# Kernel optimization log

Measured on AMD Instinct MI355X. Metric: run time of the kernel, lower is better.

The kernel has to match this reference:

```python
import jax, jax.numpy as jnp
import numpy as np

B, C, H, W = 32, 256, 32, 32
HID, NPATH = 128, 4


def setup_inputs() -> dict:
    key = jax.random.key(0)
    ks = jax.random.split(key, 16)
    s = lambda *sh: 1.0 / np.sqrt(sh[-1])
    inp = {
        "lidar": jax.random.normal(ks[0], (B, C, H, W), jnp.float32),
        "hsi": jax.random.normal(ks[1], (B, C, H, W), jnp.float32),
        "x": jax.random.normal(ks[2], (B, C, H, W), jnp.float32),
        # shared Cross_Self_attention params
        "Wq": jax.random.normal(ks[3], (C, C), jnp.float32) * s(C, C),
        "bq": jnp.zeros((C,), jnp.float32),
        "Wk": jax.random.normal(ks[4], (C, C), jnp.float32) * s(C, C),
        "bk": jnp.zeros((C,), jnp.float32),
        "Wv": jax.random.normal(ks[5], (C, C), jnp.float32) * s(C, C),
        "bv": jnp.zeros((C,), jnp.float32),
        # 1x1 conv: [out=C, in=2C]
        "conv_w": jax.random.normal(ks[6], (C, 2 * C), jnp.float32) * s(C, 2 * C),
        "conv_b": jnp.zeros((C,), jnp.float32),
        # router MLP
        "r_w1": jax.random.normal(ks[7], (HID, 2 * C), jnp.float32) * s(HID, 2 * C),
        "r_b1": jnp.zeros((HID,), jnp.float32),
        "r_w2": jax.random.normal(ks[8], (NPATH, HID), jnp.float32) * s(NPATH, HID),
        "r_b2": jnp.zeros((NPATH,), jnp.float32),
    }
    return inp


def _cross_self_attn(xq, yv, Wq, bq, Wk, bk, Wv, bv):
    # xq, yv: [b, s, c]
    q = xq @ Wq.T + bq
    k = xq @ Wk.T + bk
    v = yv @ Wv.T + bv
    probs = jax.nn.softmax(jnp.einsum("bsc,btc->bst", q, k), axis=-1)  # [b,s,s]
    return jnp.einsum("bst,btc->bsc", probs, q * v)  # bilinear value Q*V


def reference(lidar, hsi, x, Wq, bq, Wk, bk, Wv, bv, conv_w, conv_b, r_w1, r_b1, r_w2, r_b2):
    b, c, h, w = lidar.shape
    # Router: concat channels, spatial mean pool, MLP, sigmoid
    g = jnp.concatenate([lidar, hsi], axis=1).mean(axis=(2, 3))  # [b, 2c]
    path_prob = jax.nn.sigmoid(jax.nn.relu(g @ r_w1.T + r_b1) @ r_w2.T + r_b2)

    l = lidar.reshape(b, c, h * w).transpose(0, 2, 1)  # b (h w) c
    hh = hsi.reshape(b, c, h * w).transpose(0, 2, 1)

    h_emb = _cross_self_attn(l, hh, Wq, bq, Wk, bk, Wv, bv)  # [b, hw, c]
    l_emb = _cross_self_attn(hh, l, Wq, bq, Wk, bk, Wv, bv)

    h_emb = h_emb.transpose(0, 2, 1).reshape(b, c, h, w)
    l_emb = l_emb.transpose(0, 2, 1).reshape(b, c, h, w)

    cat = jnp.concatenate([l_emb, h_emb], axis=1)  # [b, 2c, h, w]
    emb = jnp.einsum("bihw,oi->bohw", cat, conv_w) + conv_b[None, :, None, None] + x
    return emb, path_prob
```

## Files before the change

kernel.cpp:

```cpp
#include <hip/hip_runtime.h>
#include <stdint.h>

typedef unsigned short u16;
typedef unsigned int u32;
typedef _Float16 f16;
typedef _Float16 f16x8 __attribute__((ext_vector_type(8)));
typedef _Float16 f16x4 __attribute__((ext_vector_type(4)));
typedef float f32x4 __attribute__((ext_vector_type(4)));

#define B_ 32
#define C_ 256
#define S_ 1024

__global__ __launch_bounds__(256) void k_mlp(
    const float* __restrict__ g,
    const float* __restrict__ w1, const float* __restrict__ b1,
    const float* __restrict__ w2, const float* __restrict__ b2,
    float* __restrict__ out)
{
    int b = blockIdx.x, tid = threadIdx.x;
    __shared__ float sg[512];
    __shared__ float sh[128];
    sg[tid]     = g[b*512 + tid]       * (1.0f/1024.0f);
    sg[tid+256] = g[b*512 + 256 + tid] * (1.0f/1024.0f);
    __syncthreads();
    if (tid < 128){
        float a = b1[tid];
        const float* w = w1 + (size_t)tid*512;
        #pragma unroll 4
        for (int k = 0; k < 512; k += 4){
            float4 wv = *(const float4*)(w + k);
            a += sg[k]*wv.x + sg[k+1]*wv.y + sg[k+2]*wv.z + sg[k+3]*wv.w;
        }
        sh[tid] = fmaxf(a, 0.f);
    }
    __syncthreads();
    if (tid < 4){
        float a = b2[tid];
        const float* w = w2 + (size_t)tid*128;
        for (int k = 0; k < 128; ++k) a += sh[k]*w[k];
        out[(size_t)8388608 + b*4 + tid] = 1.f/(1.f+expf(-a));
    }
}

__global__ __launch_bounds__(256) void k_cvtw(
    const float* __restrict__ Wq, const float* __restrict__ Wk,
    const float* __restrict__ Wv, const float* __restrict__ cw,
    f16* __restrict__ Wqf, f16* __restrict__ Wkf,
    f16* __restrict__ Wvf, f16* __restrict__ cwf)
{
    int i = (blockIdx.x*256 + threadIdx.x) * 4;
    const float* src; f16* dst; int off;
    if (i < 65536){ src = Wq; dst = Wqf; off = i; }
    else if (i < 131072){ src = Wk; dst = Wkf; off = i - 65536; }
    else if (i < 196608){ src = Wv; dst = Wvf; off = i - 131072; }
    else { src = cw; dst = cwf; off = i - 196608; }
    float4 v = *(const float4*)(src + off);
    f16x4 r = { (f16)v.x, (f16)v.y, (f16)v.z, (f16)v.w };
    *(f16x4*)(dst + off) = r;
}

__global__ __launch_bounds__(256) void k_cvt(
    const float* __restrict__ lidar, const float* __restrict__ hsi,
    f16* __restrict__ lidT, f16* __restrict__ hsiT,
    float* __restrict__ g)
{
    int z = blockIdx.z, which = z >> 5, b = z & 31;
    const float* src = (which ? hsi : lidar) + (size_t)b*C_*S_;
    f16* dst = (which ? hsiT : lidT) + (size_t)b*S_*C_;
    int tid = threadIdx.x;
    int c4 = blockIdx.y*64 + (tid&15)*4;
    int s4 = blockIdx.x*64 + (tid>>4)*4;
    float4 m[4];
    #pragma unroll
    for (int r = 0; r < 4; ++r) m[r] = *(const float4*)(src + (size_t)(c4+r)*S_ + s4);
    f16x4 t0 = { (f16)m[0].x, (f16)m[1].x, (f16)m[2].x, (f16)m[3].x };
    f16x4 t1 = { (f16)m[0].y, (f16)m[1].y, (f16)m[2].y, (f16)m[3].y };
    f16x4 t2 = { (f16)m[0].z, (f16)m[1].z, (f16)m[2].z, (f16)m[3].z };
    f16x4 t3 = { (f16)m[0].w, (f16)m[1].w, (f16)m[2].w, (f16)m[3].w };
    *(f16x4*)(dst + (size_t)(s4+0)*C_ + c4) = t0;
    *(f16x4*)(dst + (size_t)(s4+1)*C_ + c4) = t1;
    *(f16x4*)(dst + (size_t)(s4+2)*C_ + c4) = t2;
    *(f16x4*)(dst + (size_t)(s4+3)*C_ + c4) = t3;
    float ps[4];
    #pragma unroll
    for (int r = 0; r < 4; ++r){
        ps[r] = m[r].x + m[r].y + m[r].z + m[r].w;
        ps[r] += __shfl_xor(ps[r], 16, 64);
        ps[r] += __shfl_xor(ps[r], 32, 64);
    }
    __shared__ float sred[4][64];
    int wv = tid>>6, lane = tid&63;
    if ((lane>>4) == 0){
        #pragma unroll
        for (int r = 0; r < 4; ++r) sred[wv][(lane&15)*4 + r] = ps[r];
    }
    __syncthreads();
    if (tid < 64){
        float v = sred[0][tid] + sred[1][tid] + sred[2][tid] + sred[3][tid];
        atomicAdd(&g[b*512 + which*256 + blockIdx.y*64 + tid], v);
    }
}

__global__ __launch_bounds__(256) void k_qkv(
    const f16* __restrict__ lidT, const f16* __restrict__ hsiT,
    const f16* __restrict__ Wqf, const f16* __restrict__ Wkf, const f16* __restrict__ Wvf,
    const float* __restrict__ bq, const float* __restrict__ bk, const float* __restrict__ bv,
    f16* __restrict__ Qf_l, f16* __restrict__ Kf_l,
    f16* __restrict__ Qf_h, f16* __restrict__ Kf_h,
    f16* __restrict__ Qt_l, f16* __restrict__ Qt_h,
    f16* __restrict__ Vt_l, f16* __restrict__ Vt_h)
{
    int z = blockIdx.z, combo = z >> 5, b = z & 31, ww = combo % 3;
    const f16* In = ((combo < 3) ? lidT : hsiT) + (size_t)b*S_*C_;
    const f16* Wf = (ww==0) ? Wqf : (ww==1) ? Wkf : Wvf;
    const float* bias = (ww==0) ? bq : (ww==1) ? bk : bv;
    int s0 = blockIdx.x*64, o0 = blockIdx.y*64;
    int tid = threadIdx.x, w = tid>>6, lane = tid&63, quad = lane>>4, l15 = lane&15;

    __shared__ __align__(16) f16 sA[64*72];
    __shared__ __align__(16) f16 sB[64*72];

    f32x4 D[4];
    #pragma unroll
    for (int i = 0; i < 4; ++i) D[i] = (f32x4){0.f,0.f,0.f,0.f};

    int row = tid>>2, c16 = (tid&3)*16;
    for (int c0 = 0; c0 < 256; c0 += 64){
        __syncthreads();
        *(f16x8*)&sA[row*72 + c16]     = *(const f16x8*)(In + (size_t)(s0+row)*C_ + c0 + c16);
        *(f16x8*)&sA[row*72 + c16 + 8] = *(const f16x8*)(In + (size_t)(s0+row)*C_ + c0 + c16 + 8);
        *(f16x8*)&sB[row*72 + c16]     = *(const f16x8*)(Wf + (size_t)(o0+row)*C_ + c0 + c16);
        *(f16x8*)&sB[row*72 + c16 + 8] = *(const f16x8*)(Wf + (size_t)(o0+row)*C_ + c0 + c16 + 8);
        __syncthreads();
        #pragma unroll
        for (int sub = 0; sub < 2; ++sub){
            f16x8 a = *(const f16x8*)&sA[(w*16+l15)*72 + sub*32 + quad*8];
            #pragma unroll
            for (int bt = 0; bt < 4; ++bt){
                f16x8 bb = *(const f16x8*)&sB[(bt*16+l15)*72 + sub*32 + quad*8];
                D[bt] = __builtin_amdgcn_mfma_f32_16x16x32_f16(a, bb, D[bt], 0,0,0);
            }
        }
    }
    float bi[4];
    #pragma unroll
    for (int bt = 0; bt < 4; ++bt) bi[bt] = bias[o0 + bt*16 + l15];

    if (ww == 0){
        f16* F = ((combo==0) ? Qf_l : Qf_h) + (size_t)b*S_*C_;
        #pragma unroll
        for (int bt = 0; bt < 4; ++bt)
            #pragma unroll
            for (int r = 0; r < 4; ++r)
                F[(size_t)(s0 + w*16 + quad*4 + r)*C_ + o0 + bt*16 + l15] = (f16)(D[bt][r] + bi[bt]);
    } else if (ww == 1){
        f16* F = ((combo==1) ? Kf_l : Kf_h) + (size_t)b*S_*C_;
        #pragma unroll
        for (int bt = 0; bt < 4; ++bt)
            #pragma unroll
            for (int r = 0; r < 4; ++r)
                F[(size_t)(s0 + w*16 + quad*4 + r)*C_ + o0 + bt*16 + l15] = (f16)(D[bt][r] + bi[bt]);
    }
    if (ww != 1){
        __syncthreads();
        #pragma unroll
        for (int bt = 0; bt < 4; ++bt)
            #pragma unroll
            for (int r = 0; r < 4; ++r)
                sA[(bt*16+l15)*72 + w*16 + quad*4 + r] = (f16)(D[bt][r] + bi[bt]);
        __syncthreads();
        f16* T = (combo==0) ? Qt_l : (combo==3) ? Qt_h : (combo==2) ? Vt_l : Vt_h;
        T += (size_t)b*C_*S_;
        int o_r = tid>>2, s16b = (tid&3)*16;
        *(f16x8*)(T + (size_t)(o0+o_r)*S_ + s0 + s16b)     = *(const f16x8*)&sA[o_r*72 + s16b];
        *(f16x8*)(T + (size_t)(o0+o_r)*S_ + s0 + s16b + 8) = *(const f16x8*)&sA[o_r*72 + s16b + 8];
    }
}

__global__ __launch_bounds__(256) void k_qv(
    const f16* __restrict__ Qt_l, const f16* __restrict__ Qt_h,
    const f16* __restrict__ Vt_l, const f16* __restrict__ Vt_h,
    f16* __restrict__ QVT1, f16* __restrict__ QVT2)
{
    size_t idx = (size_t)(blockIdx.x*256 + threadIdx.x) * 8;
    f16x8 a = *(const f16x8*)(Qt_l+idx);
    f16x8 b = *(const f16x8*)(Vt_h+idx);
    *(f16x8*)(QVT1+idx) = a*b;
    f16x8 c = *(const f16x8*)(Qt_h+idx);
    f16x8 d = *(const f16x8*)(Vt_l+idx);
    *(f16x8*)(QVT2+idx) = c*d;
}

__global__ __launch_bounds__(256, 2) void k_attn(
    const f16* __restrict__ Qf_l, const f16* __restrict__ Kf_l,
    const f16* __restrict__ Qf_h, const f16* __restrict__ Kf_h,
    const f16* __restrict__ QVT1, const f16* __restrict__ QVT2,
    f16* __restrict__ cat)
{
    int inst = blockIdx.y;
    int b = inst >> 1, which = inst & 1;
    const f16* Qf  = (which ? Qf_h : Qf_l) + (size_t)b*S_*C_;
    const f16* Kf  = (which ? Kf_h : Kf_l) + (size_t)b*S_*C_;
    const f16* QVT = (which ? QVT2 : QVT1) + (size_t)b*C_*S_;
    f16* outp = cat + (size_t)b*S_*512 + (which ? 0 : 256);
    int s0 = blockIdx.x*64;
    int tid = threadIdx.x, w = tid>>6, lane = tid&63, quad = lane>>4, l15 = lane&15;

    __shared__ __align__(16) f16 sK[64*264];
    __shared__ __align__(16) f16 sV[256*72];
    __shared__ __align__(16) f16 sPw[4][16*66];

    f16x8 qa[8];
    {
        const f16* qrow = Qf + (size_t)(s0 + w*16 + l15)*C_ + quad*8;
        #pragma unroll
        for (int i = 0; i < 8; ++i) qa[i] = *(const f16x8*)(qrow + i*32);
    }
    float mrun[4], lrun[4];
    #pragma unroll
    for (int r = 0; r < 4; ++r){ mrun[r] = -1e30f; lrun[r] = 0.f; }
    f32x4 pacc[16];
    #pragma unroll
    for (int i = 0; i < 16; ++i) pacc[i] = (f32x4){0.f,0.f,0.f,0.f};

    for (int tt = 0; tt < 16; ++tt){
        int t0 = tt*64;
        __syncthreads();
        #pragma unroll
        for (int p = 0; p < 8; ++p){
            int idx = p*256 + tid;
            int row = idx >> 5, c8 = (idx & 31)*8;
            *(f16x8*)&sK[row*264 + c8] = *(const f16x8*)(Kf + (size_t)(t0+row)*C_ + c8);
        }
        #pragma unroll
        for (int p = 0; p < 8; ++p){
            int idx = p*256 + tid;
            int row = idx >> 3, t8 = (idx & 7)*8;
            *(f16x8*)&sV[row*72 + t8] = *(const f16x8*)(QVT + (size_t)row*S_ + t0 + t8);
        }
        __syncthreads();

        f32x4 sacc[4];
        #pragma unroll
        for (int bt = 0; bt < 4; ++bt) sacc[bt] = (f32x4){0.f,0.f,0.f,0.f};
        #pragma unroll
        for (int ks = 0; ks < 8; ++ks){
            #pragma unroll
            for (int bt = 0; bt < 4; ++bt){
                f16x8 kb = *(const f16x8*)&sK[(bt*16+l15)*264 + ks*32 + quad*8];
                sacc[bt] = __builtin_amdgcn_mfma_f32_16x16x32_f16(qa[ks], kb, sacc[bt], 0,0,0);
            }
        }

        float alpha[4], lsum[4];
        #pragma unroll
        for (int r = 0; r < 4; ++r){
            float tm = fmaxf(fmaxf(sacc[0][r], sacc[1][r]), fmaxf(sacc[2][r], sacc[3][r]));
            #pragma unroll
            for (int off = 1; off < 16; off <<= 1) tm = fmaxf(tm, __shfl_xor(tm, off, 64));
            float mn = fmaxf(mrun[r], tm);
            alpha[r] = __expf(mrun[r] - mn);
            mrun[r] = mn;
            float acc = 0.f;
            #pragma unroll
            for (int bt = 0; bt < 4; ++bt){
                float p = __expf(sacc[bt][r] - mn);
                sPw[w][(quad*4+r)*66 + bt*16 + l15] = (f16)p;
                acc += p;
            }
            #pragma unroll
            for (int off = 1; off < 16; off <<= 1) acc += __shfl_xor(acc, off, 64);
            lsum[r] = acc;
            lrun[r] = lrun[r]*alpha[r] + lsum[r];
        }
        #pragma unroll
        for (int cf = 0; cf < 16; ++cf)
            #pragma unroll
            for (int r = 0; r < 4; ++r) pacc[cf][r] *= alpha[r];

        f16x8 pa0 = *(const f16x8*)&sPw[w][l15*66 + quad*8];
        f16x8 pa1 = *(const f16x8*)&sPw[w][l15*66 + 32 + quad*8];

        #pragma unroll
        for (int cf = 0; cf < 16; ++cf){
            f16x8 vb0 = *(const f16x8*)&sV[(cf*16+l15)*72 + quad*8];
            f16x8 vb1 = *(const f16x8*)&sV[(cf*16+l15)*72 + 32 + quad*8];
            pacc[cf] = __builtin_amdgcn_mfma_f32_16x16x32_f16(pa0, vb0, pacc[cf], 0,0,0);
            pacc[cf] = __builtin_amdgcn_mfma_f32_16x16x32_f16(pa1, vb1, pacc[cf], 0,0,0);
        }
    }

    #pragma unroll
    for (int r = 0; r < 4; ++r){
        int s = w*16 + quad*4 + r;
        float rl = 1.f / lrun[r];
        #pragma unroll
        for (int cf = 0; cf < 16; ++cf)
            outp[(size_t)(s0+s)*512 + cf*16 + l15] = (f16)(pacc[cf][r] * rl);
    }
}

__global__ __launch_bounds__(256) void k_conv(
    const f16* __restrict__ cat, const f16* __restrict__ cwf,
    const float* __restrict__ cb, const float* __restrict__ x,
    float* __restrict__ out)
{
    int b = blockIdx.z;
    int s0 = blockIdx.x*64, o0 = blockIdx.y*64;
    int tid = threadIdx.x, w = tid>>6, lane = tid&63, quad = lane>>4, l15 = lane&15;

    __shared__ __align__(16) f16 sA[64*72];
    __shared__ __align__(16) f16 sB[64*72];

    f32x4 D[4];
    #pragma unroll
    for (int i = 0; i < 4; ++i) D[i] = (f32x4){0.f,0.f,0.f,0.f};

    const f16* catb = cat + (size_t)b*S_*512;
    int row = tid>>2, c16 = (tid&3)*16;
    for (int i0 = 0; i0 < 512; i0 += 64){
        __syncthreads();
        *(f16x8*)&sA[row*72 + c16]     = *(const f16x8*)(cwf + (size_t)(o0+row)*512 + i0 + c16);
        *(f16x8*)&sA[row*72 + c16 + 8] = *(const f16x8*)(cwf + (size_t)(o0+row)*512 + i0 + c16 + 8);
        *(f16x8*)&sB[row*72 + c16]     = *(const f16x8*)(catb + (size_t)(s0+row)*512 + i0 + c16);
        *(f16x8*)&sB[row*72 + c16 + 8] = *(const f16x8*)(catb + (size_t)(s0+row)*512 + i0 + c16 + 8);
        __syncthreads();
        #pragma unroll
        for (int sub = 0; sub < 2; ++sub){
            f16x8 a = *(const f16x8*)&sA[(w*16+l15)*72 + sub*32 + quad*8];
            #pragma unroll
            for (int bt = 0; bt < 4; ++bt){
                f16x8 bb = *(const f16x8*)&sB[(bt*16+l15)*72 + sub*32 + quad*8];
                D[bt] = __builtin_amdgcn_mfma_f32_16x16x32_f16(a, bb, D[bt], 0,0,0);
            }
        }
    }
    #pragma unroll
    for (int r = 0; r < 4; ++r){
        int o_loc = w*16 + quad*4 + r;
        float cbv = cb[o0 + o_loc];
        size_t base = (size_t)b*C_*S_ + (size_t)(o0+o_loc)*S_ + s0;
        #pragma unroll
        for (int bt = 0; bt < 4; ++bt){
            size_t a = base + bt*16 + l15;
            out[a] = D[bt][r] + cbv + x[a];
        }
    }
}

extern "C" void kernel_launch(void* const* d_in, const int* in_sizes, int n_in,
                              void* d_out, int out_size, void* d_ws, size_t ws_size,
                              hipStream_t stream)
{
    const float* lidar = (const float*)d_in[0];
    const float* hsi   = (const float*)d_in[1];
    const float* x     = (const float*)d_in[2];
    const float* Wq = (const float*)d_in[3];  const float* bq = (const float*)d_in[4];
    const float* Wk = (const float*)d_in[5];  const float* bk = (const float*)d_in[6];
    const float* Wv = (const float*)d_in[7];  const float* bv = (const float*)d_in[8];
    const float* cw = (const float*)d_in[9];  const float* cb = (const float*)d_in[10];
    const float* rw1 = (const float*)d_in[11]; const float* rb1 = (const float*)d_in[12];
    const float* rw2 = (const float*)d_in[13]; const float* rb2 = (const float*)d_in[14];
    float* outF = (float*)d_out;
    char* ws = (char*)d_ws;
    const size_t M = 1ull<<20;

    f16* lidT = (f16*)(ws +   0*M);
    f16* hsiT = (f16*)(ws +  16*M);
    f16* Qf_l = (f16*)(ws +  32*M);
    f16* Kf_l = (f16*)(ws +  48*M);
    f16* Qf_h = (f16*)(ws +  64*M);
    f16* Kf_h = (f16*)(ws +  80*M);
    f16* Qt_l = (f16*)(ws +  96*M);
    f16* Qt_h = (f16*)(ws + 112*M);
    f16* cat  = (f16*)(ws + 128*M);
    float* g  = (float*)(ws + 160*M);
    f16* Wqf  = (f16*)(ws + 161*M);
    f16* Wkf  = (f16*)(ws + 161*M + 131072);
    f16* Wvf  = (f16*)(ws + 161*M + 262144);
    f16* cwf  = (f16*)(ws + 161*M + 393216);
    f16* QVT1 = lidT;
    f16* QVT2 = hsiT;
    f16* Vt_l = (f16*)d_out;
    f16* Vt_h = (f16*)d_out + 8388608;

    hipMemsetAsync(g, 0, 4096*sizeof(float), stream);
    k_cvtw<<<320, 256, 0, stream>>>(Wq, Wk, Wv, cw, Wqf, Wkf, Wvf, cwf);
    k_cvt<<<dim3(16,4,64), 256, 0, stream>>>(lidar, hsi, lidT, hsiT, g);
    k_mlp<<<32, 256, 0, stream>>>(g, rw1, rb1, rw2, rb2, outF);
    k_qkv<<<dim3(16,4,192), 256, 0, stream>>>(lidT, hsiT, Wqf, Wkf, Wvf, bq, bk, bv,
                                              Qf_l, Kf_l, Qf_h, Kf_h, Qt_l, Qt_h, Vt_l, Vt_h);
    k_qv<<<4096, 256, 0, stream>>>(Qt_l, Qt_h, Vt_l, Vt_h, QVT1, QVT2);
    k_attn<<<dim3(16,64), 256, 0, stream>>>(Qf_l, Kf_l, Qf_h, Kf_h, QVT1, QVT2, cat);
    k_conv<<<dim3(16,4,32), 256, 0, stream>>>(cat, cwf, cb, x, outF);
}
```

Baseline: 407.4 us.

## Rework attention with 32x32 MFMA split tiles and enlarge QKV/conv GEMM tiles

The attention kernel now uses 32x32x16 MFMA, with waves splitting a 64x64 score tile two ways over query rows and key columns. K fragments are loaded straight from global memory into registers instead of going through shared memory. Softmax max and sum are reduced across waves through shared memory, and the output is staged through LDS for coalesced stores. The QKV and conv GEMMs double their tile along one dimension (128 rows) so each wave issues two MFMA chains per B fragment, halving grid size and increasing register use. In exchange, the attention kernel adds several extra block-wide barriers per key tile and carries more register pressure.

```diff
diff --git a/kernel.cpp b/kernel.cpp
--- a/kernel.cpp
+++ b/kernel.cpp
@@ -7,6 +7,7 @@
 typedef _Float16 f16x8 __attribute__((ext_vector_type(8)));
 typedef _Float16 f16x4 __attribute__((ext_vector_type(4)));
 typedef float f32x4 __attribute__((ext_vector_type(4)));
+typedef float f32x16 __attribute__((ext_vector_type(16)));
 
 #define B_ 32
 #define C_ 256
@@ -115,31 +116,38 @@
     const f16* In = ((combo < 3) ? lidT : hsiT) + (size_t)b*S_*C_;
     const f16* Wf = (ww==0) ? Wqf : (ww==1) ? Wkf : Wvf;
     const float* bias = (ww==0) ? bq : (ww==1) ? bk : bv;
-    int s0 = blockIdx.x*64, o0 = blockIdx.y*64;
+    int s0 = blockIdx.x*128, o0 = blockIdx.y*64;
     int tid = threadIdx.x, w = tid>>6, lane = tid&63, quad = lane>>4, l15 = lane&15;
 
-    __shared__ __align__(16) f16 sA[64*72];
+    __shared__ __align__(16) f16 sA[128*72];
     __shared__ __align__(16) f16 sB[64*72];
 
-    f32x4 D[4];
-    #pragma unroll
-    for (int i = 0; i < 4; ++i) D[i] = (f32x4){0.f,0.f,0.f,0.f};
-
-    int row = tid>>2, c16 = (tid&3)*16;
+    f32x4 D[2][4];
+    #pragma unroll
+    for (int h = 0; h < 2; ++h)
+        #pragma unroll
+        for (int i = 0; i < 4; ++i) D[h][i] = (f32x4){0.f,0.f,0.f,0.f};
+
+    int rowA = tid>>1, cA = (tid&1)*32;
+    int rowB = tid>>2, cB = (tid&3)*16;
     for (int c0 = 0; c0 < 256; c0 += 64){
         __syncthreads();
-        *(f16x8*)&sA[row*72 + c16]     = *(const f16x8*)(In + (size_t)(s0+row)*C_ + c0 + c16);
-        *(f16x8*)&sA[row*72 + c16 + 8] = *(const f16x8*)(In + (size_t)(s0+row)*C_ + c0 + c16 + 8);
-        *(f16x8*)&sB[row*72 + c16]     = *(const f16x8*)(Wf + (size_t)(o0+row)*C_ + c0 + c16);
-        *(f16x8*)&sB[row*72 + c16 + 8] = *(const f16x8*)(Wf + (size_t)(o0+row)*C_ + c0 + c16 + 8);
+        #pragma unroll
+        for (int j = 0; j < 4; ++j)
+            *(f16x8*)&sA[rowA*72 + cA + 8*j] = *(const f16x8*)(In + (size_t)(s0+rowA)*C_ + c0 + cA + 8*j);
+        #pragma unroll
+        for (int j = 0; j < 2; ++j)
+            *(f16x8*)&sB[rowB*72 + cB + 8*j] = *(const f16x8*)(Wf + (size_t)(o0+rowB)*C_ + c0 + cB + 8*j);
         __syncthreads();
         #pragma unroll
         for (int sub = 0; sub < 2; ++sub){
-            f16x8 a = *(const f16x8*)&sA[(w*16+l15)*72 + sub*32 + quad*8];
+            f16x8 a0 = *(const f16x8*)&sA[(w*16+l15)*72 + sub*32 + quad*8];
+            f16x8 a1 = *(const f16x8*)&sA[((w+4)*16+l15)*72 + sub*32 + quad*8];
             #pragma unroll
             for (int bt = 0; bt < 4; ++bt){
                 f16x8 bb = *(const f16x8*)&sB[(bt*16+l15)*72 + sub*32 + quad*8];
-                D[bt] = __builtin_amdgcn_mfma_f32_16x16x32_f16(a, bb, D[bt], 0,0,0);
+                D[0][bt] = __builtin_amdgcn_mfma_f32_16x16x32_f16(a0, bb, D[0][bt], 0,0,0);
+                D[1][bt] = __builtin_amdgcn_mfma_f32_16x16x32_f16(a1, bb, D[1][bt], 0,0,0);
             }
         }
     }
@@ -147,34 +155,33 @@
     #pragma unroll
     for (int bt = 0; bt < 4; ++bt) bi[bt] = bias[o0 + bt*16 + l15];
 
-    if (ww == 0){
-        f16* F = ((combo==0) ? Qf_l : Qf_h) + (size_t)b*S_*C_;
-        #pragma unroll
-        for (int bt = 0; bt < 4; ++bt)
-            #pragma unroll
-            for (int r = 0; r < 4; ++r)
-                F[(size_t)(s0 + w*16 + quad*4 + r)*C_ + o0 + bt*16 + l15] = (f16)(D[bt][r] + bi[bt]);
-    } else if (ww == 1){
-        f16* F = ((combo==1) ? Kf_l : Kf_h) + (size_t)b*S_*C_;
-        #pragma unroll
-        for (int bt = 0; bt < 4; ++bt)
-            #pragma unroll
-            for (int r = 0; r < 4; ++r)
-                F[(size_t)(s0 + w*16 + quad*4 + r)*C_ + o0 + bt*16 + l15] = (f16)(D[bt][r] + bi[bt]);
+    if (ww != 2){
+        f16* F = (ww==0) ? ((combo==0) ? Qf_l : Qf_h) : ((combo==1) ? Kf_l : Kf_h);
+        F += (size_t)b*S_*C_;
+        #pragma unroll
+        for (int h = 0; h < 2; ++h)
+            #pragma unroll
+            for (int bt = 0; bt < 4; ++bt)
+                #pragma unroll
+                for (int r = 0; r < 4; ++r)
+                    F[(size_t)(s0 + h*64 + w*16 + quad*4 + r)*C_ + o0 + bt*16 + l15] = (f16)(D[h][bt][r] + bi[bt]);
     }
     if (ww != 1){
         __syncthreads();
         #pragma unroll
-        for (int bt = 0; bt < 4; ++bt)
-            #pragma unroll
-            for (int r = 0; r < 4; ++r)
-                sA[(bt*16+l15)*72 + w*16 + quad*4 + r] = (f16)(D[bt][r] + bi[bt]);
+        for (int h = 0; h < 2; ++h)
+            #pragma unroll
+            for (int bt = 0; bt < 4; ++bt)
+                #pragma unroll
+                for (int r = 0; r < 4; ++r)
+                    sA[(bt*16+l15)*136 + h*64 + w*16 + quad*4 + r] = (f16)(D[h][bt][r] + bi[bt]);
         __syncthreads();
         f16* T = (combo==0) ? Qt_l : (combo==3) ? Qt_h : (combo==2) ? Vt_l : Vt_h;
         T += (size_t)b*C_*S_;
-        int o_r = tid>>2, s16b = (tid&3)*16;
-        *(f16x8*)(T + (size_t)(o0+o_r)*S_ + s0 + s16b)     = *(const f16x8*)&sA[o_r*72 + s16b];
-        *(f16x8*)(T + (size_t)(o0+o_r)*S_ + s0 + s16b + 8) = *(const f16x8*)&sA[o_r*72 + s16b + 8];
+        int o_r = tid>>2, sc = (tid&3)*32;
+        #pragma unroll
+        for (int j = 0; j < 4; ++j)
+            *(f16x8*)(T + (size_t)(o0+o_r)*S_ + s0 + sc + 8*j) = *(const f16x8*)&sA[o_r*136 + sc + 8*j];
     }
 }
 
@@ -205,99 +212,112 @@
     const f16* QVT = (which ? QVT2 : QVT1) + (size_t)b*C_*S_;
     f16* outp = cat + (size_t)b*S_*512 + (which ? 0 : 256);
     int s0 = blockIdx.x*64;
-    int tid = threadIdx.x, w = tid>>6, lane = tid&63, quad = lane>>4, l15 = lane&15;
-
-    __shared__ __align__(16) f16 sK[64*264];
+    int tid = threadIdx.x, w = tid>>6, lane = tid&63;
+    int l31 = lane&31, b5 = lane>>5;
+    int sh2 = w&1, hf = w>>1;
+
     __shared__ __align__(16) f16 sV[256*72];
-    __shared__ __align__(16) f16 sPw[4][16*66];
-
-    f16x8 qa[8];
+    __shared__ __align__(16) f16 sP[64*72];
+    __shared__ float sRm[2][64], sRl[2][64];
+    __shared__ float sSt[64][2];
+
+    f16x8 qB[16];
     {
-        const f16* qrow = Qf + (size_t)(s0 + w*16 + l15)*C_ + quad*8;
-        #pragma unroll
-        for (int i = 0; i < 8; ++i) qa[i] = *(const f16x8*)(qrow + i*32);
-    }
-    float mrun[4], lrun[4];
-    #pragma unroll
-    for (int r = 0; r < 4; ++r){ mrun[r] = -1e30f; lrun[r] = 0.f; }
-    f32x4 pacc[16];
-    #pragma unroll
-    for (int i = 0; i < 16; ++i) pacc[i] = (f32x4){0.f,0.f,0.f,0.f};
+        const f16* qbase = Qf + (size_t)(s0 + 32*sh2 + l31)*C_ + b5*8;
+        #pragma unroll
+        for (int k = 0; k < 16; ++k) qB[k] = *(const f16x8*)(qbase + k*16);
+    }
+    if (tid < 64){ sSt[tid][0] = -1e30f; sSt[tid][1] = 0.f; }
+
+    f32x16 pacc[4];
+    #pragma unroll
+    for (int i = 0; i < 4; ++i) pacc[i] = (f32x16)(0.f);
+
+    const f16* kbase = Kf + (size_t)(32*hf + l31)*C_ + b5*8;
+    int smy = 32*sh2 + l31;
 
     for (int tt = 0; tt < 16; ++tt){
         int t0 = tt*64;
         __syncthreads();
         #pragma unroll
         for (int p = 0; p < 8; ++p){
-            int idx = p*256 + tid;
-            int row = idx >> 5, c8 = (idx & 31)*8;
-            *(f16x8*)&sK[row*264 + c8] = *(const f16x8*)(Kf + (size_t)(t0+row)*C_ + c8);
-        }
-        #pragma unroll
-        for (int p = 0; p < 8; ++p){
-            int idx = p*256 + tid;
-            int row = idx >> 3, t8 = (idx & 7)*8;
+            int idx = p*256 + tid; int row = idx>>3, t8 = (idx&7)*8;
             *(f16x8*)&sV[row*72 + t8] = *(const f16x8*)(QVT + (size_t)row*S_ + t0 + t8);
         }
-        __syncthreads();
-
-        f32x4 sacc[4];
-        #pragma unroll
-        for (int bt = 0; bt < 4; ++bt) sacc[bt] = (f32x4){0.f,0.f,0.f,0.f};
-        #pragma unroll
-        for (int ks = 0; ks < 8; ++ks){
-            #pragma unroll
-            for (int bt = 0; bt < 4; ++bt){
-                f16x8 kb = *(const f16x8*)&sK[(bt*16+l15)*264 + ks*32 + quad*8];
-                sacc[bt] = __builtin_amdgcn_mfma_f32_16x16x32_f16(qa[ks], kb, sacc[bt], 0,0,0);
+        f16x8 kA[16];
+        {
+            const f16* kb = kbase + (size_t)t0*C_;
+            #pragma unroll
+            for (int k = 0; k < 16; ++k) kA[k] = *(const f16x8*)(kb + k*16);
+        }
+        __syncthreads();
+
+        f32x16 St = (f32x16)(0.f);
+        #pragma unroll
+        for (int k = 0; k < 16; ++k)
+            St = __builtin_amdgcn_mfma_f32_32x32x16_f16(kA[k], qB[k], St, 0,0,0);
+
+        float tmax = St[0];
+        #pragma unroll
+        for (int i = 1; i < 16; ++i) tmax = fmaxf(tmax, St[i]);
+        tmax = fmaxf(tmax, __shfl_xor(tmax, 32, 64));
+        if (lane < 32) sRm[hf][32*sh2 + lane] = tmax;
+        __syncthreads();
+
+        float mo = sSt[smy][0];
+        float mn = fmaxf(mo, fmaxf(sRm[0][smy], sRm[1][smy]));
+        float p16[16];
+        float ls = 0.f;
+        #pragma unroll
+        for (int i = 0; i < 16; ++i){ p16[i] = __expf(St[i] - mn); ls += p16[i]; }
+        #pragma unroll
+        for (int g = 0; g < 4; ++g){
+            f16x4 pk = { (f16)p16[4*g], (f16)p16[4*g+1], (f16)p16[4*g+2], (f16)p16[4*g+3] };
+            *(f16x4*)&sP[smy*72 + 32*hf + 8*g + 4*b5] = pk;
+        }
+        ls += __shfl_xor(ls, 32, 64);
+        if (lane < 32) sRl[hf][32*sh2 + lane] = ls;
+        __syncthreads();
+
+        float alpha = __expf(mo - mn);
+        if (hf == 0 && lane < 32){
+            float ln = sSt[smy][1]*alpha + sRl[0][smy] + sRl[1][smy];
+            sSt[smy][0] = mn; sSt[smy][1] = ln;
+        }
+        #pragma unroll
+        for (int ct = 0; ct < 4; ++ct)
+            #pragma unroll
+            for (int i = 0; i < 16; ++i) pacc[ct][i] *= alpha;
+
+        #pragma unroll
+        for (int kp = 0; kp < 4; ++kp){
+            f16x8 pB = *(const f16x8*)&sP[smy*72 + kp*16 + b5*8];
+            #pragma unroll
+            for (int ct = 0; ct < 4; ++ct){
+                f16x8 vA = *(const f16x8*)&sV[(128*hf + 32*ct + l31)*72 + kp*16 + b5*8];
+                pacc[ct] = __builtin_amdgcn_mfma_f32_32x32x16_f16(vA, pB, pacc[ct], 0,0,0);
             }
         }
-
-        float alpha[4], lsum[4];
-        #pragma unroll
-        for (int r = 0; r < 4; ++r){
-            float tm = fmaxf(fmaxf(sacc[0][r], sacc[1][r]), fmaxf(sacc[2][r], sacc[3][r]));
-            #pragma unroll
-            for (int off = 1; off < 16; off <<= 1) tm = fmaxf(tm, __shfl_xor(tm, off, 64));
-            float mn = fmaxf(mrun[r], tm);
-            alpha[r] = __expf(mrun[r] - mn);
-            mrun[r] = mn;
-            float acc = 0.f;
-            #pragma unroll
-            for (int bt = 0; bt < 4; ++bt){
-                float p = __expf(sacc[bt][r] - mn);
-                sPw[w][(quad*4+r)*66 + bt*16 + l15] = (f16)p;
-                acc += p;
-            }
-            #pragma unroll
-            for (int off = 1; off < 16; off <<= 1) acc += __shfl_xor(acc, off, 64);
-            lsum[r] = acc;
-            lrun[r] = lrun[r]*alpha[r] + lsum[r];
-        }
-        #pragma unroll
-        for (int cf = 0; cf < 16; ++cf)
-            #pragma unroll
-            for (int r = 0; r < 4; ++r) pacc[cf][r] *= alpha[r];
-
-        f16x8 pa0 = *(const f16x8*)&sPw[w][l15*66 + quad*8];
-        f16x8 pa1 = *(const f16x8*)&sPw[w][l15*66 + 32 + quad*8];
-
-        #pragma unroll
-        for (int cf = 0; cf < 16; ++cf){
-            f16x8 vb0 = *(const f16x8*)&sV[(cf*16+l15)*72 + quad*8];
-            f16x8 vb1 = *(const f16x8*)&sV[(cf*16+l15)*72 + 32 + quad*8];
-            pacc[cf] = __builtin_amdgcn_mfma_f32_16x16x32_f16(pa0, vb0, pacc[cf], 0,0,0);
-            pacc[cf] = __builtin_amdgcn_mfma_f32_16x16x32_f16(pa1, vb1, pacc[cf], 0,0,0);
-        }
-    }
-
-    #pragma unroll
-    for (int r = 0; r < 4; ++r){
-        int s = w*16 + quad*4 + r;
-        float rl = 1.f / lrun[r];
-        #pragma unroll
-        for (int cf = 0; cf < 16; ++cf)
-            outp[(size_t)(s0+s)*512 + cf*16 + l15] = (f16)(pacc[cf][r] * rl);
+    }
+
+    __syncthreads();
+    float rl = 1.f / sSt[smy][1];
+    f16* sE = sV;
+    #pragma unroll
+    for (int ct = 0; ct < 4; ++ct)
+        #pragma unroll
+        for (int i = 0; i < 16; ++i){
+            int cl = 128*hf + 32*ct + (i&3) + 8*(i>>2) + 4*b5;
+            sE[(32*sh2 + l31)*264 + cl] = (f16)(pacc[ct][i] * rl);
+        }
+    __syncthreads();
+    {
+        int s = tid>>2;
+        #pragma unroll
+        for (int i = 0; i < 8; ++i){
+            int c8 = ((tid&3) + 4*i)*8;
+            *(f16x8*)(outp + (size_t)(s0+s)*512 + c8) = *(const f16x8*)&sE[s*264 + c8];
+        }
     }
 }
 
@@ -307,46 +327,55 @@
     float* __restrict__ out)
 {
     int b = blockIdx.z;
-    int s0 = blockIdx.x*64, o0 = blockIdx.y*64;
+    int s0 = blockIdx.x*64, o0 = blockIdx.y*128;
     int tid = threadIdx.x, w = tid>>6, lane = tid&63, quad = lane>>4, l15 = lane&15;
 
-    __shared__ __align__(16) f16 sA[64*72];
+    __shared__ __align__(16) f16 sA[128*72];
     __shared__ __align__(16) f16 sB[64*72];
 
-    f32x4 D[4];
-    #pragma unroll
-    for (int i = 0; i < 4; ++i) D[i] = (f32x4){0.f,0.f,0.f,0.f};
+    f32x4 D[2][4];
+    #pragma unroll
+    for (int h = 0; h < 2; ++h)
+        #pragma unroll
+        for (int i = 0; i < 4; ++i) D[h][i] = (f32x4){0.f,0.f,0.f,0.f};
 
     const f16* catb = cat + (size_t)b*S_*512;
-    int row = tid>>2, c16 = (tid&3)*16;
+    int rowA = tid>>1, iA = (tid&1)*32;
+    int rowB = tid>>2, iB = (tid&3)*16;
     for (int i0 = 0; i0 < 512; i0 += 64){
         __syncthreads();
-        *(f16x8*)&sA[row*72 + c16]     = *(const f16x8*)(cwf + (size_t)(o0+row)*512 + i0 + c16);
-        *(f16x8*)&sA[row*72 + c16 + 8] = *(const f16x8*)(cwf + (size_t)(o0+row)*512 + i0 + c16 + 8);
-        *(f16x8*)&sB[row*72 + c16]     = *(const f16x8*)(catb + (size_t)(s0+row)*512 + i0 + c16);
-        *(f16x8*)&sB[row*72 + c16 + 8] = *(const f16x8*)(catb + (size_t)(s0+row)*512 + i0 + c16 + 8);
+        #pragma unroll
+        for (int j = 0; j < 4; ++j)
+            *(f16x8*)&sA[rowA*72 + iA + 8*j] = *(const f16x8*)(cwf + (size_t)(o0+rowA)*512 + i0 + iA + 8*j);
+        #pragma unroll
+        for (int j = 0; j < 2; ++j)
+            *(f16x8*)&sB[rowB*72 + iB + 8*j] = *(const f16x8*)(catb + (size_t)(s0+rowB)*512 + i0 + iB + 8*j);
         __syncthreads();
         #pragma unroll
         for (int sub = 0; sub < 2; ++sub){
-            f16x8 a = *(const f16x8*)&sA[(w*16+l15)*72 + sub*32 + quad*8];
+            f16x8 a0 = *(const f16x8*)&sA[(w*16+l15)*72 + sub*32 + quad*8];
+            f16x8 a1 = *(const f16x8*)&sA[((w+4)*16+l15)*72 + sub*32 + quad*8];
             #pragma unroll
             for (int bt = 0; bt < 4; ++bt){
                 f16x8 bb = *(const f16x8*)&sB[(bt*16+l15)*72 + sub*32 + quad*8];
-                D[bt] = __builtin_amdgcn_mfma_f32_16x16x32_f16(a, bb, D[bt], 0,0,0);
+                D[0][bt] = __builtin_amdgcn_mfma_f32_16x16x32_f16(a0, bb, D[0][bt], 0,0,0);
+                D[1][bt] = __builtin_amdgcn_mfma_f32_16x16x32_f16(a1, bb, D[1][bt], 0,0,0);
             }
         }
     }
     #pragma unroll
-    for (int r = 0; r < 4; ++r){
-        int o_loc = w*16 + quad*4 + r;
-        float cbv = cb[o0 + o_loc];
-        size_t base = (size_t)b*C_*S_ + (size_t)(o0+o_loc)*S_ + s0;
-        #pragma unroll
-        for (int bt = 0; bt < 4; ++bt){
-            size_t a = base + bt*16 + l15;
-            out[a] = D[bt][r] + cbv + x[a];
-        }
-    }
+    for (int h = 0; h < 2; ++h)
+        #pragma unroll
+        for (int r = 0; r < 4; ++r){
+            int o_loc = h*64 + w*16 + quad*4 + r;
+            float cbv = cb[o0 + o_loc];
+            size_t base = (size_t)b*C_*S_ + (size_t)(o0+o_loc)*S_ + s0;
+            #pragma unroll
+            for (int bt = 0; bt < 4; ++bt){
+                size_t a = base + bt*16 + l15;
+                out[a] = D[h][bt][r] + cbv + x[a];
+            }
+        }
 }
 
 extern "C" void kernel_launch(void* const* d_in, const int* in_sizes, int n_in,
@@ -389,9 +418,9 @@
     k_cvtw<<<320, 256, 0, stream>>>(Wq, Wk, Wv, cw, Wqf, Wkf, Wvf, cwf);
     k_cvt<<<dim3(16,4,64), 256, 0, stream>>>(lidar, hsi, lidT, hsiT, g);
     k_mlp<<<32, 256, 0, stream>>>(g, rw1, rb1, rw2, rb2, outF);
-    k_qkv<<<dim3(16,4,192), 256, 0, stream>>>(lidT, hsiT, Wqf, Wkf, Wvf, bq, bk, bv,
-                                              Qf_l, Kf_l, Qf_h, Kf_h, Qt_l, Qt_h, Vt_l, Vt_h);
+    k_qkv<<<dim3(8,4,192), 256, 0, stream>>>(lidT, hsiT, Wqf, Wkf, Wvf, bq, bk, bv,
+                                             Qf_l, Kf_l, Qf_h, Kf_h, Qt_l, Qt_h, Vt_l, Vt_h);
     k_qv<<<4096, 256, 0, stream>>>(Qt_l, Qt_h, Vt_l, Vt_h, QVT1, QVT2);
     k_attn<<<dim3(16,64), 256, 0, stream>>>(Qf_l, Kf_l, Qf_h, Kf_h, QVT1, QVT2, cat);
-    k_conv<<<dim3(16,4,32), 256, 0, stream>>>(cat, cwf, cb, x, outF);
-}
+    k_conv<<<dim3(16,2,32), 256, 0, stream>>>(cat, cwf, cb, x, outF);
+}
```

Result: slower. 438.4 us (+7.6%).
